# Performance work log

Measured on AMD Instinct MI355X. Metric: run time of the kernel, lower is better.

Reference implementation:

```python
import jax, jax.numpy as jnp
import numpy as np


def setup_inputs() -> dict:
    key = jax.random.key(0)
    k1, k2 = jax.random.split(key)
    B, N, D = 4, 4096, 3
    set1 = jax.random.normal(k1, (B, N, D), dtype=jnp.float32)
    set2 = jax.random.normal(k2, (B, N, D), dtype=jnp.float32)
    return {"set1": set1, "set2": set2}


def reference(set1, set2):
    # set1: [B, N, d], set2: [B, M, d]
    # Pairwise Euclidean distances via the Gram-matrix identity
    x2 = jnp.sum(set1 * set1, axis=-1)                    # [B, N]
    y2 = jnp.sum(set2 * set2, axis=-1)                    # [B, M]
    xy = jnp.einsum('bnd,bmd->bnm', set1, set2)           # [B, N, M]
    d2 = jnp.maximum(x2[:, :, None] + y2[:, None, :] - 2.0 * xy, 0.0)
    dist = jnp.sqrt(d2)                                   # [B, N, M]
    term1 = jnp.mean(jnp.min(dist, axis=2), axis=1)       # mean over N of row mins
    term2 = jnp.mean(jnp.min(dist, axis=1), axis=1)       # mean over M of col mins
    # per-instance sum, then average over batch (matches ahd / instance_num)
    return jnp.mean(term1 + term2)
```

## Files before the change

### kernel.cpp

```cpp
#include <hip/hip_runtime.h>
#include <math.h>

#define BATCH 4
#define NPTS  4096
#define RPB   256
#define ROWS  4
#define ROWS_PER_BLOCK (RPB * ROWS)
#define CHUNKS (NPTS / ROWS_PER_BLOCK)
#define SEGS  32
#define SEG_LEN (NPTS / SEGS)

#define RED_BLOCKS 128
#define FP_SCALE   268435456.0


__global__ __launch_bounds__(RPB) void ahd_min_kernel(
    const float* __restrict__ set1, const float* __restrict__ set2,
    float* __restrict__ part, unsigned long long* __restrict__ total,
    unsigned int* __restrict__ counter)
{
    if (blockIdx.x == 0 && blockIdx.y == 0 && blockIdx.z == 0 && threadIdx.x == 0) {
        *total = 0ULL;
        *counter = 0u;
    }

    const int dir      = blockIdx.z;
    const int b        = blockIdx.y;
    const int rowChunk = blockIdx.x / SEGS;
    const int seg      = blockIdx.x % SEGS;

    const float* __restrict__ X = dir ? set2 : set1;
    const float* __restrict__ Y = dir ? set1 : set2;

    __shared__ float4 ys[SEG_LEN];

    const float* ybase = Y + ((size_t)b * NPTS + (size_t)seg * SEG_LEN) * 3;
    for (int i = threadIdx.x; i < SEG_LEN; i += RPB) {
        const float y0 = ybase[i * 3 + 0];
        const float y1 = ybase[i * 3 + 1];
        const float y2 = ybase[i * 3 + 2];
        ys[i] = make_float4(y0, y1, y2, fmaf(y0, y0, fmaf(y1, y1, y2 * y2)));
    }
    __syncthreads();

    float nx0[ROWS], nx1[ROWS], nx2[ROWS], hx[ROWS], acc[ROWS];
    const int rowBase = rowChunk * ROWS_PER_BLOCK + threadIdx.x;
    #pragma unroll
    for (int r = 0; r < ROWS; ++r) {
        const float* xp = X + ((size_t)b * NPTS + rowBase + r * RPB) * 3;
        const float x0 = xp[0], x1 = xp[1], x2 = xp[2];
        nx0[r] = -2.0f * x0;
        nx1[r] = -2.0f * x1;
        nx2[r] = -2.0f * x2;
        hx[r]  = fmaf(x0, x0, fmaf(x1, x1, x2 * x2));
        acc[r] = 3.4e38f;
    }

    #pragma unroll 4
    for (int j = 0; j < SEG_LEN; ++j) {
        const float4 y = ys[j];
        #pragma unroll
        for (int r = 0; r < ROWS; ++r) {
            const float q = fmaf(nx0[r], y.x,
                            fmaf(nx1[r], y.y,
                            fmaf(nx2[r], y.z, y.w)));
            acc[r] = fminf(acc[r], q);
        }
    }

    float* dst = part + (((size_t)(dir * BATCH + b) * SEGS + seg) * NPTS);
    #pragma unroll
    for (int r = 0; r < ROWS; ++r)
        dst[rowBase + r * RPB] = fmaxf(acc[r] + hx[r], 0.0f);
}

__global__ __launch_bounds__(RPB) void ahd_reduce_kernel(
    const float* __restrict__ part, unsigned long long* __restrict__ total,
    unsigned int* __restrict__ counter, float* __restrict__ out)
{
    const int g    = blockIdx.x * RPB + threadIdx.x;
    const int dirb = g >> 12;
    const int n    = g & (NPTS - 1);

    const float* p = part + ((size_t)dirb * SEGS) * NPTS + n;
    float m = p[0];
    #pragma unroll
    for (int s = 1; s < SEGS; ++s)
        m = fminf(m, p[(size_t)s * NPTS]);

    float d = sqrtf(m);

    #pragma unroll
    for (int off = 32; off > 0; off >>= 1)
        d += __shfl_down(d, off, 64);

    __shared__ unsigned long long ws[4];
    const int lane = threadIdx.x & 63;
    const int w    = threadIdx.x >> 6;
    if (lane == 0)
        ws[w] = (unsigned long long)((double)d * FP_SCALE);
    __syncthreads();

    if (threadIdx.x == 0) {
        const unsigned long long bs = ws[0] + ws[1] + ws[2] + ws[3];
        atomicAdd(total, bs);
        __threadfence();
        const unsigned int cnt = atomicAdd(counter, 1u);
        if (cnt == (unsigned int)(gridDim.x - 1)) {
            const unsigned long long fin = atomicAdd(total, 0ULL);
            out[0] = (float)((double)fin * (1.0 / FP_SCALE)
                             * (1.0 / (double)(BATCH * NPTS)));
        }
    }
}

extern "C" void kernel_launch(void* const* d_in, const int* in_sizes, int n_in,
                              void* d_out, int out_size, void* d_ws, size_t ws_size,
                              hipStream_t stream) {
    const float* set1 = (const float*)d_in[0];
    const float* set2 = (const float*)d_in[1];
    float* out = (float*)d_out;

    unsigned long long* total = (unsigned long long*)d_ws;
    unsigned int* counter = (unsigned int*)((char*)d_ws + 8);
    float* part = (float*)((char*)d_ws + 64);

    dim3 grid(CHUNKS * SEGS, BATCH, 2);
    ahd_min_kernel<<<grid, dim3(RPB), 0, stream>>>(set1, set2, part, total, counter);
    ahd_reduce_kernel<<<RED_BLOCKS, dim3(RPB), 0, stream>>>(part, total, counter, out);
}
```

Before: 24.65 us.

## Replace per-segment partial buffer with atomicMin into a single min array

The per-segment partial-minimum buffer (32 segments per row) is replaced by one min array per point, combined with integer atomicMin on the float bit pattern, which is order-preserving for non-negative floats. An init kernel sets the array to all-ones and zeroes the counters. The reduce kernel now reads one uint4 per thread instead of 32 strided loads, cutting partial-buffer writes and reads by a factor of 32. In exchange it adds an extra kernel launch and atomic contention (32 writers per address), and the inner loop unroll goes from 4 to 8.

```diff
diff --git a/kernel.cpp b/kernel.cpp
--- a/kernel.cpp
+++ b/kernel.cpp
@@ -10,20 +10,23 @@
 #define SEGS  32
 #define SEG_LEN (NPTS / SEGS)
 
-#define RED_BLOCKS 128
-#define FP_SCALE   268435456.0
+#define NMINS (2 * BATCH * NPTS)
+#define FP_SCALE 268435456.0
 
+
+__global__ __launch_bounds__(RPB) void ahd_init(
+    uint4* __restrict__ mins4, unsigned long long* __restrict__ total,
+    unsigned int* __restrict__ counter)
+{
+    const int i = blockIdx.x * RPB + threadIdx.x;
+    mins4[i] = make_uint4(0xFFFFFFFFu, 0xFFFFFFFFu, 0xFFFFFFFFu, 0xFFFFFFFFu);
+    if (i == 0) { *total = 0ULL; *counter = 0u; }
+}
 
 __global__ __launch_bounds__(RPB) void ahd_min_kernel(
     const float* __restrict__ set1, const float* __restrict__ set2,
-    float* __restrict__ part, unsigned long long* __restrict__ total,
-    unsigned int* __restrict__ counter)
+    unsigned int* __restrict__ mins)
 {
-    if (blockIdx.x == 0 && blockIdx.y == 0 && blockIdx.z == 0 && threadIdx.x == 0) {
-        *total = 0ULL;
-        *counter = 0u;
-    }
-
     const int dir      = blockIdx.z;
     const int b        = blockIdx.y;
     const int rowChunk = blockIdx.x / SEGS;
@@ -56,7 +59,7 @@
         acc[r] = 3.4e38f;
     }
 
-    #pragma unroll 4
+    #pragma unroll 8
     for (int j = 0; j < SEG_LEN; ++j) {
         const float4 y = ys[j];
         #pragma unroll
@@ -68,27 +71,22 @@
         }
     }
 
-    float* dst = part + (((size_t)(dir * BATCH + b) * SEGS + seg) * NPTS);
+    unsigned int* base = mins + (size_t)dir * BATCH * NPTS + (size_t)b * NPTS;
     #pragma unroll
-    for (int r = 0; r < ROWS; ++r)
-        dst[rowBase + r * RPB] = fmaxf(acc[r] + hx[r], 0.0f);
+    for (int r = 0; r < ROWS; ++r) {
+        const float d2 = fmaxf(acc[r] + hx[r], 0.0f);
+        atomicMin(&base[rowBase + r * RPB], __float_as_uint(d2));
+    }
 }
 
 __global__ __launch_bounds__(RPB) void ahd_reduce_kernel(
-    const float* __restrict__ part, unsigned long long* __restrict__ total,
+    const uint4* __restrict__ mins4, unsigned long long* __restrict__ total,
     unsigned int* __restrict__ counter, float* __restrict__ out)
 {
-    const int g    = blockIdx.x * RPB + threadIdx.x;
-    const int dirb = g >> 12;
-    const int n    = g & (NPTS - 1);
-
-    const float* p = part + ((size_t)dirb * SEGS) * NPTS + n;
-    float m = p[0];
-    #pragma unroll
-    for (int s = 1; s < SEGS; ++s)
-        m = fminf(m, p[(size_t)s * NPTS]);
-
-    float d = sqrtf(m);
+    const int i = blockIdx.x * RPB + threadIdx.x;
+    const uint4 v = mins4[i];
+    float d = sqrtf(__uint_as_float(v.x)) + sqrtf(__uint_as_float(v.y))
+            + sqrtf(__uint_as_float(v.z)) + sqrtf(__uint_as_float(v.w));
 
     #pragma unroll
     for (int off = 32; off > 0; off >>= 1)
@@ -123,9 +121,12 @@
 
     unsigned long long* total = (unsigned long long*)d_ws;
     unsigned int* counter = (unsigned int*)((char*)d_ws + 8);
-    float* part = (float*)((char*)d_ws + 64);
+    unsigned int* mins = (unsigned int*)((char*)d_ws + 64);
 
+    ahd_init<<<NMINS / (4 * RPB), dim3(RPB), 0, stream>>>(
+        (uint4*)mins, total, counter);
     dim3 grid(CHUNKS * SEGS, BATCH, 2);
-    ahd_min_kernel<<<grid, dim3(RPB), 0, stream>>>(set1, set2, part, total, counter);
-    ahd_reduce_kernel<<<RED_BLOCKS, dim3(RPB), 0, stream>>>(part, total, counter, out);
+    ahd_min_kernel<<<grid, dim3(RPB), 0, stream>>>(set1, set2, mins);
+    ahd_reduce_kernel<<<NMINS / (4 * RPB), dim3(RPB), 0, stream>>>(
+        (const uint4*)mins, total, counter, out);
 }
```

Result: no change. 24.69 us (+0.2%).
